# Optimization experiments

Measured on AMD Instinct MI355X. Metric: run time of the kernel, lower is better.

Reference implementation:

```python
import jax, jax.numpy as jnp
import numpy as np

HID = 256
B, H, W, Q = 4, 192, 192, 36864


def conv3x3(x, w, b):
    # x [B,C,H,W], w [O,C,3,3]
    y = jax.lax.conv_general_dilated(x, w, (1, 1), ((1, 1), (1, 1)),
                                     dimension_numbers=('NCHW', 'OIHW', 'NCHW'))
    return y + b[None, :, None, None]


def gather_nchw(x, iy, ix):
    # nearest-neighbor gather: x [B,C,H,W], iy/ix [B,Q] -> [B,Q,C]
    b, c, h, w = x.shape
    lin = iy * w + ix
    g = jnp.take_along_axis(x.reshape(b, c, h * w), lin[:, None, :], axis=2)
    return jnp.transpose(g, (0, 2, 1))


def bilinear_border(x, cy, cx):
    # grid_sample bilinear, padding_mode='border', align_corners=False
    b, c, h, w = x.shape
    fy = ((cy + 1.0) * h - 1.0) * 0.5
    fx = ((cx + 1.0) * w - 1.0) * 0.5
    y0 = jnp.floor(fy)
    x0 = jnp.floor(fx)
    wy = fy - y0
    wx = fx - x0
    y0i = jnp.clip(y0, 0, h - 1).astype(jnp.int32)
    y1i = jnp.clip(y0 + 1, 0, h - 1).astype(jnp.int32)
    x0i = jnp.clip(x0, 0, w - 1).astype(jnp.int32)
    x1i = jnp.clip(x0 + 1, 0, w - 1).astype(jnp.int32)
    v00 = gather_nchw(x, y0i, x0i)
    v01 = gather_nchw(x, y0i, x1i)
    v10 = gather_nchw(x, y1i, x0i)
    v11 = gather_nchw(x, y1i, x1i)
    wy = wy[..., None]
    wx = wx[..., None]
    return (v00 * (1 - wy) * (1 - wx) + v01 * (1 - wy) * wx
            + v10 * wy * (1 - wx) + v11 * wy * wx)


def setup_inputs():
    key = jax.random.key(0)
    ks = jax.random.split(key, 20)
    sc = 0.05
    d = {}
    d['inp'] = jax.random.normal(ks[0], (B, 3, H, W), jnp.float32)
    d['score'] = jax.random.normal(ks[1], (B, 3, H, W), jnp.float32)
    d['coord'] = jax.random.uniform(ks[2], (B, Q, 2), jnp.float32, -1.0, 1.0)
    d['cell'] = jnp.full((B, Q, 2), 2.0 / H, jnp.float32)
    d['coef_w'] = jax.random.normal(ks[3], (HID, 9, 3, 3), jnp.float32) * sc
    d['coef_b'] = jnp.zeros((HID,), jnp.float32)
    d['freq_w'] = jax.random.normal(ks[4], (HID, 9, 3, 3), jnp.float32) * sc
    d['freq_b'] = jnp.zeros((HID,), jnp.float32)
    d['phase_w'] = jax.random.normal(ks[5], (HID // 2, 2), jnp.float32) * sc  # Linear(2, HID//2, bias=False)
    d['a1_w'] = jax.random.normal(ks[6], (128, 3, 3, 3), jnp.float32) * sc
    d['a1_b'] = jnp.zeros((128,), jnp.float32)
    d['a2_w'] = jax.random.normal(ks[7], (3, 128, 3, 3), jnp.float32) * sc
    d['a2_b'] = jnp.zeros((3,), jnp.float32)
    dims = [HID, 256, 256, 256, 256, 3]
    for i in range(5):
        d[f'im_w{i}'] = jax.random.normal(ks[8 + i], (dims[i + 1], dims[i]), jnp.float32) * sc
        d[f'im_b{i}'] = jnp.zeros((dims[i + 1],), jnp.float32)
    return d


def lte_forward(inp, score, coord, cell,
                coef_w, coef_b, freq_w, freq_b, phase_w,
                a1_w, a1_b, a2_w, a2_b,
                im_w0, im_b0, im_w1, im_b1, im_w2, im_b2, im_w3, im_b3, im_w4, im_b4):
    # adapter: conv -> sin -> conv -> sin (Sine w0=1)
    weights = jnp.sin(conv3x3(jnp.sin(conv3x3(inp, a1_w, a1_b)), a2_w, a2_b))
    feat = jnp.concatenate([inp, score, weights], axis=1)  # [B,9,H,W]
    coef = conv3x3(feat, coef_w, coef_b)  # [B,HID,H,W]
    freq = conv3x3(feat, freq_w, freq_b)
    h, w = feat.shape[-2], feat.shape[-1]
    eps = 1e-6
    # single ensemble member (vx=vy=0): clamp coord and nearest-sample
    cy = jnp.clip(coord[..., 0], -1 + eps, 1 - eps)
    cx = jnp.clip(coord[..., 1], -1 + eps, 1 - eps)
    iy = jnp.clip(jnp.round(((cy + 1.0) * h - 1.0) * 0.5), 0, h - 1).astype(jnp.int32)
    ix = jnp.clip(jnp.round(((cx + 1.0) * w - 1.0) * 0.5), 0, w - 1).astype(jnp.int32)
    q_coef = gather_nchw(coef, iy, ix)  # [B,Q,HID]
    q_freq = gather_nchw(freq, iy, ix)  # [B,Q,HID]
    # nearest pixel-center coordinates (make_coord values)
    qy = -1.0 + (2.0 * iy.astype(jnp.float32) + 1.0) / h
    qx = -1.0 + (2.0 * ix.astype(jnp.float32) + 1.0) / w
    rel = jnp.stack([(coord[..., 0] - qy) * h, (coord[..., 1] - qx) * w], axis=-1)  # [B,Q,2]
    rel_cell = cell * jnp.asarray([h, w], jnp.float32)
    # split into (even,odd) frequency pairs: [B,Q,HID/2,2], contract with rel_coord
    qf = q_freq.reshape(q_freq.shape[0], q_freq.shape[1], HID // 2, 2)
    qf = jnp.einsum('bqjk,bqk->bqj', qf, rel)  # [B,Q,HID/2]
    qf = qf + jnp.einsum('bqk,jk->bqj', rel_cell, phase_w)  # phase linear, no bias
    qf = jnp.concatenate([jnp.cos(jnp.pi * qf), jnp.sin(jnp.pi * qf)], axis=-1)  # [B,Q,HID]
    x = q_coef * qf
    for lw, lb in ((im_w0, im_b0), (im_w1, im_b1), (im_w2, im_b2), (im_w3, im_b3)):
        x = jax.nn.relu(jnp.einsum('bqi,oi->bqo', x, lw) + lb)
    pred = jnp.einsum('bqi,oi->bqo', x, im_w4) + im_b4  # [B,Q,3]
    area = jnp.abs(rel[..., 0] * rel[..., 1]) + 1e-9
    ret = pred * (area / area)[..., None]  # single member -> weight 1 (kept for fidelity)
    ret = ret + bilinear_border(inp, coord[..., 0], coord[..., 1])
    return ret


def reference(inp, score, coord, cell,
              coef_w, coef_b, freq_w, freq_b, phase_w,
              a1_w, a1_b, a2_w, a2_b,
              im_w0, im_b0, im_w1, im_b1, im_w2, im_b2, im_w3, im_b3, im_w4, im_b4):
    return lte_forward(inp, score, coord, cell,
                       coef_w, coef_b, freq_w, freq_b, phase_w,
                       a1_w, a1_b, a2_w, a2_b,
                       im_w0, im_b0, im_w1, im_b1, im_w2, im_b2, im_w3, im_b3, im_w4, im_b4)
```

## Files before the change

kernel.cpp:

```cpp
#include <hip/hip_runtime.h>

typedef unsigned short u16;
typedef unsigned int   u32;
typedef unsigned long long u64;
typedef __attribute__((ext_vector_type(8))) short v8s;
typedef __attribute__((ext_vector_type(8))) unsigned short v8u;
typedef __attribute__((ext_vector_type(4))) float v4f;

#define PI_F 3.14159265358979323846f

__device__ __forceinline__ float bf2f(u16 v){ u32 u = ((u32)v) << 16; return __builtin_bit_cast(float, u); }
__device__ __forceinline__ u16 f2bf(float f){
    u32 u = __builtin_bit_cast(u32, f);
    u32 r = (u + 0x7fffu + ((u >> 16) & 1u)) >> 16;
    return (u16)r;
}
__device__ __forceinline__ bool is_f32(const void* cellp){
    u32 u = *(const u32*)cellp;
    return ((u >> 16) != (u & 0xffffu));
}
__device__ __forceinline__ float ldin(const void* p, int i, bool f32){
    return f32 ? ((const float*)p)[i] : bf2f(((const u16*)p)[i]);
}

#define FEAT16_OFF 0
#define W2P_OFF   4718592
#define A1W_OFF   4816896
#define A1B_OFF   4830720
#define A2W_OFF   4831232
#define A2B_OFF   4845056
#define PWF_OFF   4845312
#define IBF_OFF   4846336
#define IWC_OFF   4850688
#define CBP_OFF   5376512
#define W4P_OFF   5378560
#define W1SW_OFF  5386752
#define W2SW_OFF  5403136

__global__ __launch_bounds__(256) void k_pack(
    const void* cw, const void* fw, const void* a1w, const void* a1b,
    const void* a2w, const void* a2b, const void* cb, const void* fb, const void* pwp,
    const void* iw0, const void* ib0, const void* iw1, const void* ib1,
    const void* iw2, const void* ib2, const void* iw3, const void* ib3,
    const void* iw4, const void* ib4, const void* cellp, char* ws){
    bool f32 = is_f32(cellp);
    u16*   w2p  = (u16*)(ws + W2P_OFF);
    float* a1wf = (float*)(ws + A1W_OFF);
    float* a1bf = (float*)(ws + A1B_OFF);
    float* a2wf = (float*)(ws + A2W_OFF);
    float* a2bf = (float*)(ws + A2B_OFF);
    float* pwf  = (float*)(ws + PWF_OFF);
    float* ibf  = (float*)(ws + IBF_OFF);
    u16*   iwc  = (u16*)(ws + IWC_OFF);
    float* cbp  = (float*)(ws + CBP_OFF);
    u16*   w4p  = (u16*)(ws + W4P_OFF);
    u16*   w1sw = (u16*)(ws + W1SW_OFF);
    u16*   w2sw = (u16*)(ws + W2SW_OFF);

    int t = blockIdx.x*256 + threadIdx.x;
    if (t < 49152){
        int c = t >> 9, rem = t & 511;
        int tile = c/3, ks = c%3;
        int lm = rem >> 5, r2 = rem & 31, quad = r2 >> 3, jj = r2 & 7;
        int n = tile*16 + lm;
        int r = quad*8 + jj;
        u16 v = 0;
        if (r < 27){
            int pix = r/9, ch = r%9;
            int tap = ks*3 + pix;
            int src = ch*9 + tap;
            if (n < 256) v = f2bf(ldin(cw, n*81 + src, f32));
            else { int u_ = n - 256; int tt = u_ >> 4, nn = u_ & 15;
                   int f = 2*((tt>>1)*16 + nn) + (tt & 1);
                   v = f2bf(ldin(fw, f*81 + src, f32)); }
        }
        w2p[t] = v; return;
    }
    t -= 49152;
    if (t < 3456){ a1wf[t] = ldin(a1w, t, f32); return; }
    t -= 3456;
    if (t < 128){ a1bf[t] = ldin(a1b, t, f32); return; }
    t -= 128;
    if (t < 3456){
        int o = t/1152, r = t%1152, c = r/9, tap = r%9;
        a2wf[(o*9 + tap)*128 + c] = ldin(a2w, t, f32); return;
    }
    t -= 3456;
    if (t < 3){ a2bf[t] = ldin(a2b, t, f32); return; }
    t -= 3;
    if (t < 256){ pwf[t] = ldin(pwp, t, f32); return; }
    t -= 256;
    if (t < 1027){
        const void* src = (t < 256) ? ib0 : (t < 512) ? ib1 : (t < 768) ? ib2 : (t < 1024) ? ib3 : ib4;
        int idx = (t < 1024) ? (t & 255) : (t - 1024);
        ibf[t] = ldin(src, idx, f32); return;
    }
    t -= 1027;
    if (t < 262144){
        int c = t >> 9, rem = t & 511;
        int lm = rem >> 5, r2 = rem & 31, quad = r2 >> 3, jj = r2 & 7;
        int nt = c & 3, ks = (c >> 2) & 7, wv = (c >> 5) & 3, l = c >> 7;
        int col = wv*64 + nt*16 + lm;
        int k = ks*32 + quad*8 + jj;
        const void* src = (l==0) ? iw0 : (l==1) ? iw1 : (l==2) ? iw2 : iw3;
        iwc[t] = f2bf(ldin(src, col*256 + k, f32)); return;
    }
    t -= 262144;
    if (t < 768){ return; }
    t -= 768;
    if (t < 512){
        float v;
        if (t < 256) v = ldin(cb, t, f32);
        else { int u_ = t - 256; int tt = u_ >> 4, nn = u_ & 15;
               int f = 2*((tt>>1)*16 + nn) + (tt & 1); v = ldin(fb, f, f32); }
        cbp[t] = v; return;
    }
    t -= 512;
    if (t < 4096){
        int ks = t >> 9, rem = t & 511;
        int lm = rem >> 5, r2 = rem & 31, quad = r2 >> 3, jj = r2 & 7;
        int k = ks*32 + quad*8 + jj;
        w4p[t] = (lm < 3) ? f2bf(ldin(iw4, lm*256 + k, f32)) : (u16)0;
        return;
    }
    t -= 4096;
    if (t < 8192){
        int c = t >> 9, rem = t & 511;
        int lm = rem >> 5, r2 = rem & 31, quad = r2 >> 3, jj = r2 & 7;
        int h = c >> 3, nt = (c & 7) >> 1, ks = c & 1;
        int ch = h*64 + nt*16 + lm;
        int kk = quad*8 + jj;
        u16 v = 0;
        int jr = -1, r = 0;
        if (ks == 0){ jr = kk >> 4; r = kk & 15; }
        else if (kk < 16){ jr = 2; r = kk; }
        if (jr >= 0 && r < 12){
            int px = r >> 2, ci = r & 3;
            if (ci < 3) v = f2bf(ldin(a1w, ch*27 + ci*9 + jr*3 + px, f32));
        }
        w1sw[t] = v; return;
    }
    t -= 8192;
    if (t < 18432){
        int c = t >> 9, rem = t & 511;
        int lm = rem >> 5, r2 = rem & 31, quad = r2 >> 3, jj = r2 & 7;
        int h = c / 18, tap = (c % 18) >> 1, ks = c & 1;
        int k = ks*32 + quad*8 + jj;
        int ch = h*64 + k;
        u16 v = 0;
        if (lm < 3) v = f2bf(ldin(a2w, lm*1152 + ch*9 + tap, f32));
        w2sw[t] = v; return;
    }
}

__global__ __launch_bounds__(256, 3) void k_adapter(const void* __restrict__ inp, const void* __restrict__ score,
                                                    const void* __restrict__ cellp, char* __restrict__ ws){
    __shared__ __attribute__((aligned(16))) char smem[46480];
    bool f32 = is_f32(cellp);
    const float* a1bf = (const float*)(ws + A1B_OFF);
    const float* a2bf = (const float*)(ws + A2B_OFF);
    const u16*   w1sw = (const u16*)(ws + W1SW_OFF);
    const u16*   w2sw = (const u16*)(ws + W2SW_OFF);
    u16* feat16 = (u16*)(ws + FEAT16_OFF);

    int blk = blockIdx.x; int b = blk/288; int rem = blk%288;
    int ty0 = (rem/12)*8, tx0 = (rem%12)*16;
    int tid = threadIdx.x;
    u16* S   = (u16*)smem;
    u16* A   = (u16*)(smem + 1920);
    u16* hid = (u16*)(smem + 22000);

    if (tid < 240) ((u64*)smem)[tid] = 0ULL;
    __syncthreads();
    #pragma unroll 1
    for (int e = tid; e < 720; e += 256){
        int ci = e/240, r2 = e%240, hy = r2/20, hx = r2%20;
        int gy = ty0 - 2 + hy, gx = tx0 - 2 + hx;
        if (gy >= 0 && gy < 192 && gx >= 0 && gx < 192)
            S[(hy*20+hx)*4 + ci] = f2bf(ldin(inp, (b*3+ci)*36864 + gy*192 + gx, f32));
    }
    __syncthreads();
    #pragma unroll 1
    for (int p = tid; p < 193; p += 256){
        u64* drow = (u64*)(A + p*52);
        if (p < 180){
            int hy = p/18, hx = p%18;
            #pragma unroll
            for (int jr = 0; jr < 3; ++jr){
                const u64* srow = (const u64*)(S + ((hy+jr)*20 + hx)*4);
                u64 v0 = srow[0], v1 = srow[1], v2 = srow[2];
                drow[jr*4+0] = v0; drow[jr*4+1] = v1; drow[jr*4+2] = v2; drow[jr*4+3] = 0ULL;
            }
            drow[12] = 0ULL;
        } else {
            #pragma unroll
            for (int k = 0; k < 13; ++k) drow[k] = 0ULL;
        }
    }
    __syncthreads();

    const int wv = tid >> 6, ln = tid & 63;
    const int lm = ln & 15, quad = ln >> 4;
    const int laneoff = lm*32 + quad*8;

    float bias2 = (lm < 3) ? a2bf[lm] : 0.f;
    v4f acc2[2];
    acc2[0] = (v4f){bias2,bias2,bias2,bias2};
    acc2[1] = acc2[0];

    #pragma unroll 1
    for (int h = 0; h < 2; ++h){
        float bias1 = a1bf[h*64 + wv*16 + lm];
        v8s B0 = *(const v8s*)(w1sw + (h*8 + wv*2 + 0)*512 + laneoff);
        v8s B1 = *(const v8s*)(w1sw + (h*8 + wv*2 + 1)*512 + laneoff);
        #pragma unroll 4
        for (int mt = 0; mt < 12; ++mt){
            const u16* ar = A + (mt*16 + lm)*52 + quad*8;
            v8s a0 = *(const v8s*)(ar);
            v8s a1 = *(const v8s*)(ar + 32);
            v4f c = (v4f){bias1,bias1,bias1,bias1};
            c = __builtin_amdgcn_mfma_f32_16x16x32_bf16(a0, B0, c, 0,0,0);
            c = __builtin_amdgcn_mfma_f32_16x16x32_bf16(a1, B1, c, 0,0,0);
            #pragma unroll
            for (int r = 0; r < 4; ++r){
                int px = mt*16 + quad*4 + r;
                if (px < 180){
                    int hy = px/18, hx = px - hy*18;
                    int gy = ty0 - 1 + hy, gx = tx0 - 1 + hx;
                    bool ok = (gy >= 0) & (gy < 192) & (gx >= 0) & (gx < 192);
                    hid[px*68 + wv*16 + lm] = ok ? f2bf(__sinf(c[r])) : (u16)0;
                }
            }
        }
        __syncthreads();
        #pragma unroll 2
        for (int tap = 0; tap < 9; ++tap){
            int ty = tap/3, tx = tap%3;
            v8s Bt0 = *(const v8s*)(w2sw + ((h*9 + tap)*2 + 0)*512 + laneoff);
            v8s Bt1 = *(const v8s*)(w2sw + ((h*9 + tap)*2 + 1)*512 + laneoff);
            #pragma unroll
            for (int i = 0; i < 2; ++i){
                int py = wv*2 + i;
                const u16* hrow = hid + ((py+ty)*18 + lm + tx)*68;
                v8s a0 = *(const v8s*)(hrow + quad*8);
                v8s a1 = *(const v8s*)(hrow + 32 + quad*8);
                acc2[i] = __builtin_amdgcn_mfma_f32_16x16x32_bf16(a0, Bt0, acc2[i], 0,0,0);
                acc2[i] = __builtin_amdgcn_mfma_f32_16x16x32_bf16(a1, Bt1, acc2[i], 0,0,0);
            }
        }
        __syncthreads();
    }
    u16* out3 = S;
    if (lm < 3){
        #pragma unroll
        for (int i = 0; i < 2; ++i)
            #pragma unroll
            for (int r = 0; r < 4; ++r){
                int m = (wv*2 + i)*16 + quad*4 + r;
                out3[m*4 + lm] = f2bf(__sinf(acc2[i][r]));
            }
    }
    __syncthreads();
    if (tid < 128){
        int py = tid >> 4, px = tid & 15;
        int gy = ty0 + py, gx = tx0 + px;
        int pi = b*3*36864 + gy*192 + gx;
        v8u lo, hi;
        lo[0] = f2bf(ldin(inp, pi, f32));
        lo[1] = f2bf(ldin(inp, pi + 36864, f32));
        lo[2] = f2bf(ldin(inp, pi + 2*36864, f32));
        lo[3] = f2bf(ldin(score, pi, f32));
        lo[4] = f2bf(ldin(score, pi + 36864, f32));
        lo[5] = f2bf(ldin(score, pi + 2*36864, f32));
        lo[6] = out3[tid*4 + 0];
        lo[7] = out3[tid*4 + 1];
        hi[0] = out3[tid*4 + 2];
        hi[1]=hi[2]=hi[3]=hi[4]=hi[5]=hi[6]=hi[7]=0;
        u16* fp = feat16 + ((b*192 + gy)*192 + gx)*16;
        *(v8u*)fp = lo;
        *(v8u*)(fp + 8) = hi;
    }
}

__global__ __launch_bounds__(256, 3) void k_mega(const char* __restrict__ ws,
                                                 const void* __restrict__ inp,
                                                 const void* __restrict__ coord,
                                                 const void* __restrict__ cellp,
                                                 void* __restrict__ out){
    __shared__ __attribute__((aligned(16))) char smem[46080];
    bool f32 = is_f32(cellp);
    const u16*   feat16 = (const u16*)(ws + FEAT16_OFF);
    const u16*   w2p    = (const u16*)(ws + W2P_OFF);
    const float* pwf    = (const float*)(ws + PWF_OFF);
    const float* ibf    = (const float*)(ws + IBF_OFF);
    const u16*   iwc    = (const u16*)(ws + IWC_OFF);
    const float* cbp    = (const float*)(ws + CBP_OFF);
    const u16*   w4p    = (const u16*)(ws + W4P_OFF);

    const int tid = threadIdx.x;
    const int qg0 = blockIdx.x * 64;
    const int b = qg0 / 36864;

    {
        int q = tid >> 2, j = tid & 3;
        int qg = qg0 + q;
        u16* ap = (u16*)(smem + 32768);
        float c0 = ldin(coord, qg*2, f32), c1 = ldin(coord, qg*2+1, f32);
        const float e = 1e-6f;
        float cy = fminf(fmaxf(c0, -1.f+e), 1.f-e);
        float cx = fminf(fmaxf(c1, -1.f+e), 1.f-e);
        int iy = (int)rintf(((cy+1.f)*192.f-1.f)*0.5f); iy = min(max(iy,0),191);
        int ix = (int)rintf(((cx+1.f)*192.f-1.f)*0.5f); ix = min(max(ix,0),191);
        if (j < 3){
            int yy = iy - 1 + j;
            bool yok = (yy >= 0) & (yy <= 191);
            union { u16 a[32]; v8u v[4]; } buf;
            #pragma unroll
            for (int c = 0; c < 32; ++c) buf.a[c] = 0;
            if (yok){
                const u16* base = feat16 + ((b*192 + yy)*192)*16;
                #pragma unroll
                for (int pix = 0; pix < 3; ++pix){
                    int xx = ix - 1 + pix;
                    if (xx >= 0 && xx <= 191){
                        const u16* s = base + xx*16;
                        v8u v = *(const v8u*)s;
                        u16 c8 = s[8];
                        #pragma unroll
                        for (int c = 0; c < 8; ++c) buf.a[pix*9+c] = v[c];
                        buf.a[pix*9+8] = c8;
                    }
                }
            }
            u16* dst = ap + q*96 + j*32;
            *(v8u*)(dst)      = buf.v[0];
            *(v8u*)(dst + 8)  = buf.v[1];
            *(v8u*)(dst + 16) = buf.v[2];
            *(v8u*)(dst + 24) = buf.v[3];
        } else {
            float qy = -1.f + (2.f*iy + 1.f)/192.f;
            float qx = -1.f + (2.f*ix + 1.f)/192.f;
            float4 mmv;
            mmv.x = (c0 - qy)*192.f; mmv.y = (c1 - qx)*192.f;
            mmv.z = ldin(cellp, qg*2, f32)*192.f; mmv.w = ldin(cellp, qg*2+1, f32)*192.f;
            ((float4*)(smem + 45056))[q] = mmv;
        }
    }
    __syncthreads();

    const int wv = tid >> 6, ln = tid & 63;
    const int lm = ln & 15, quad = ln >> 4;
    const int laneoff = lm*32 + quad*8;
    u16* X = (u16*)smem;

    {
        v8s afr[3];
        #pragma unroll
        for (int ks = 0; ks < 3; ++ks)
            afr[ks] = *(const v8s*)(smem + 32768 + ((wv*16 + lm)*96 + ks*32 + quad*8)*2);
        float4 mm[4];
        #pragma unroll
        for (int r = 0; r < 4; ++r)
            mm[r] = ((const float4*)(smem + 45056))[wv*16 + quad*4 + r];
        float p0[8], p1[8];
        #pragma unroll
        for (int g = 0; g < 8; ++g){
            int j = g*16 + lm;
            p0[g] = pwf[2*j]; p1[g] = pwf[2*j+1];
        }
        v8s Bc0[3], Bc1[3], Bf0[3], Bf1[3];
        {
            const u16* p;
            p = w2p + 0*1536  + laneoff; Bc0[0]=*(const v8s*)p; Bc0[1]=*(const v8s*)(p+512); Bc0[2]=*(const v8s*)(p+1024);
            p = w2p + 8*1536  + laneoff; Bc1[0]=*(const v8s*)p; Bc1[1]=*(const v8s*)(p+512); Bc1[2]=*(const v8s*)(p+1024);
            p = w2p + 16*1536 + laneoff; Bf0[0]=*(const v8s*)p; Bf0[1]=*(const v8s*)(p+512); Bf0[2]=*(const v8s*)(p+1024);
            p = w2p + 17*1536 + laneoff; Bf1[0]=*(const v8s*)p; Bf1[1]=*(const v8s*)(p+512); Bf1[2]=*(const v8s*)(p+1024);
        }
        #pragma unroll 1
        for (int g = 0; g < 8; ++g){
            float bb0 = cbp[g*16+lm], bb1 = cbp[(8+g)*16+lm];
            float bb2 = cbp[(16+2*g)*16+lm], bb3 = cbp[(17+2*g)*16+lm];
            v4f a0 = (v4f){bb0,bb0,bb0,bb0};
            v4f a1 = (v4f){bb1,bb1,bb1,bb1};
            v4f a2 = (v4f){bb2,bb2,bb2,bb2};
            v4f a3 = (v4f){bb3,bb3,bb3,bb3};
            #pragma unroll
            for (int ks = 0; ks < 3; ++ks){
                a0 = __builtin_amdgcn_mfma_f32_16x16x32_bf16(afr[ks], Bc0[ks], a0, 0,0,0);
                a1 = __builtin_amdgcn_mfma_f32_16x16x32_bf16(afr[ks], Bc1[ks], a1, 0,0,0);
                a2 = __builtin_amdgcn_mfma_f32_16x16x32_bf16(afr[ks], Bf0[ks], a2, 0,0,0);
                a3 = __builtin_amdgcn_mfma_f32_16x16x32_bf16(afr[ks], Bf1[ks], a3, 0,0,0);
            }
            if (g < 7){
                const u16* p;
                p = w2p + (g+1)*1536    + laneoff; Bc0[0]=*(const v8s*)p; Bc0[1]=*(const v8s*)(p+512); Bc0[2]=*(const v8s*)(p+1024);
                p = w2p + (9+g)*1536    + laneoff; Bc1[0]=*(const v8s*)p; Bc1[1]=*(const v8s*)(p+512); Bc1[2]=*(const v8s*)(p+1024);
                p = w2p + (18+2*g)*1536 + laneoff; Bf0[0]=*(const v8s*)p; Bf0[1]=*(const v8s*)(p+512); Bf0[2]=*(const v8s*)(p+1024);
                p = w2p + (19+2*g)*1536 + laneoff; Bf1[0]=*(const v8s*)p; Bf1[1]=*(const v8s*)(p+512); Bf1[2]=*(const v8s*)(p+1024);
            }
            int j = g*16 + lm;
            int koff_c = (j>>5)*2048 + (j&31);
            int koff_s = ((128+j)>>5)*2048 + (j&31);
            #pragma unroll
            for (int r = 0; r < 4; ++r){
                float qf = a2[r]*mm[r].x + a3[r]*mm[r].y + mm[r].z*p0[g] + mm[r].w*p1[g];
                float sn, cs;
                __sincosf(PI_F * qf, &sn, &cs);
                int q = wv*16 + quad*4 + r;
                X[koff_c + q*32] = f2bf(a0[r] * cs);
                X[koff_s + q*32] = f2bf(a1[r] * sn);
            }
        }
    }
    __syncthreads();

    #pragma unroll 1
    for (int l = 0; l < 4; ++l){
        const u16* Wb = iwc + (l*4 + wv)*16384 + laneoff;
        v4f acc[4][4];
        #pragma unroll
        for (int nt = 0; nt < 4; ++nt){
            float bv = ibf[l*256 + wv*64 + nt*16 + lm];
            #pragma unroll
            for (int mt = 0; mt < 4; ++mt) acc[nt][mt] = (v4f){bv,bv,bv,bv};
        }
        v8s bw[2][4];
        #pragma unroll
        for (int nt = 0; nt < 4; ++nt){
            bw[0][nt] = *(const v8s*)(Wb + (0*4 + nt)*512);
            bw[1][nt] = *(const v8s*)(Wb + (1*4 + nt)*512);
        }
        #pragma unroll
        for (int ks = 0; ks < 8; ++ks){
            v8s a[4];
            #pragma unroll
            for (int mt = 0; mt < 4; ++mt)
                a[mt] = *(const v8s*)(smem + (ks*2048 + (mt*16 + lm)*32 + quad*8)*2);
            v8s nb[4];
            if (ks < 6){
                #pragma unroll
                for (int nt = 0; nt < 4; ++nt)
                    nb[nt] = *(const v8s*)(Wb + ((ks+2)*4 + nt)*512);
            }
            #pragma unroll
            for (int nt = 0; nt < 4; ++nt)
                #pragma unroll
                for (int mt = 0; mt < 4; ++mt)
                    acc[nt][mt] = __builtin_amdgcn_mfma_f32_16x16x32_bf16(a[mt], bw[ks&1][nt], acc[nt][mt], 0,0,0);
            if (ks < 6){
                #pragma unroll
                for (int nt = 0; nt < 4; ++nt) bw[ks&1][nt] = nb[nt];
            }
        }
        __syncthreads();
        #pragma unroll
        for (int nt = 0; nt < 4; ++nt){
            int col = wv*64 + nt*16 + lm;
            u16* base = X + (col>>5)*2048 + (col&31);
            #pragma unroll
            for (int mt = 0; mt < 4; ++mt)
                #pragma unroll
                for (int r = 0; r < 4; ++r){
                    int q = mt*16 + quad*4 + r;
                    base[q*32] = f2bf(fmaxf(acc[nt][mt][r], 0.f));
                }
        }
        __syncthreads();
    }

    {
        float bv = (lm < 3) ? ibf[1024 + lm] : 0.f;
        v4f accf = (v4f){bv,bv,bv,bv};
        v8s bA = *(const v8s*)(w4p + laneoff);
        #pragma unroll
        for (int ks = 0; ks < 8; ++ks){
            v8s a = *(const v8s*)(smem + (ks*2048 + (wv*16 + lm)*32 + quad*8)*2);
            v8s bN;
            if (ks < 7) bN = *(const v8s*)(w4p + (ks+1)*512 + laneoff);
            accf = __builtin_amdgcn_mfma_f32_16x16x32_bf16(a, bA, accf, 0,0,0);
            bA = bN;
        }
        if (lm < 3){
            #pragma unroll
            for (int r = 0; r < 4; ++r){
                int q = wv*16 + quad*4 + r;
                int qg = qg0 + q;
                float c0 = ldin(coord, qg*2, f32), c1 = ldin(coord, qg*2+1, f32);
                float fy = ((c0 + 1.f)*192.f - 1.f)*0.5f;
                float fx = ((c1 + 1.f)*192.f - 1.f)*0.5f;
                float y0 = floorf(fy), x0 = floorf(fx);
                float wy = fy - y0, wx = fx - x0;
                int y0i = (int)fminf(fmaxf(y0, 0.f), 191.f);
                int y1i = (int)fminf(fmaxf(y0 + 1.f, 0.f), 191.f);
                int x0i = (int)fminf(fmaxf(x0, 0.f), 191.f);
                int x1i = (int)fminf(fmaxf(x0 + 1.f, 0.f), 191.f);
                int ibase = (b*3 + lm)*36864;
                float v00 = ldin(inp, ibase + y0i*192 + x0i, f32);
                float v01 = ldin(inp, ibase + y0i*192 + x1i, f32);
                float v10 = ldin(inp, ibase + y1i*192 + x0i, f32);
                float v11 = ldin(inp, ibase + y1i*192 + x1i, f32);
                float bil = v00*(1.f-wy)*(1.f-wx) + v01*(1.f-wy)*wx + v10*wy*(1.f-wx) + v11*wy*wx;
                float val = accf[r] + bil;
                if (f32) ((float*)out)[qg*3 + lm] = val;
                else     ((u16*)out)[qg*3 + lm] = f2bf(val);
            }
        }
    }
}

extern "C" void kernel_launch(void* const* d_in, const int* in_sizes, int n_in,
                              void* d_out, int out_size, void* d_ws, size_t ws_size,
                              hipStream_t stream){
    (void)in_sizes; (void)n_in; (void)out_size; (void)ws_size;
    const void* inp   = d_in[0];
    const void* score = d_in[1];
    const void* coord = d_in[2];
    const void* cellp = d_in[3];
    const void* cw    = d_in[4];
    const void* cb    = d_in[5];
    const void* fw    = d_in[6];
    const void* fb    = d_in[7];
    const void* pw    = d_in[8];
    const void* a1w   = d_in[9];
    const void* a1b   = d_in[10];
    const void* a2w   = d_in[11];
    const void* a2b   = d_in[12];
    const void* iw0   = d_in[13];
    const void* ib0   = d_in[14];
    const void* iw1   = d_in[15];
    const void* ib1   = d_in[16];
    const void* iw2   = d_in[17];
    const void* ib2   = d_in[18];
    const void* iw3   = d_in[19];
    const void* ib3   = d_in[20];
    const void* iw4   = d_in[21];
    const void* ib4   = d_in[22];
    char* ws = (char*)d_ws;

    hipLaunchKernelGGL(k_pack, dim3(1374), dim3(256), 0, stream,
                       cw, fw, a1w, a1b, a2w, a2b, cb, fb, pw,
                       iw0, ib0, iw1, ib1, iw2, ib2, iw3, ib3, iw4, ib4,
                       cellp, ws);
    hipLaunchKernelGGL(k_adapter, dim3(1152), dim3(256), 0, stream, inp, score, cellp, ws);
    hipLaunchKernelGGL(k_mega, dim3(2304), dim3(256), 0, stream, (const char*)ws, inp, coord, cellp, d_out);
}
```

Baseline: 313.5 us.

## Split MLP GEMM across waves by query rows instead of output columns

The hidden-layer GEMM work is redistributed: each wave now computes all 256 output columns for its own 16 query rows, where before it computed 64 columns for all 64 rows. The weight packing is reordered to match, and the B-fragment stream is double-buffered across 32 groups. This cuts LDS activation reads per wave (one A fragment per k-step instead of four). In exchange every wave streams the full weight matrix from global/L2, four times the weight traffic per block.

```diff
diff --git a/kernel.cpp b/kernel.cpp
--- a/kernel.cpp
+++ b/kernel.cpp
@@ -99,8 +99,8 @@
     if (t < 262144){
         int c = t >> 9, rem = t & 511;
         int lm = rem >> 5, r2 = rem & 31, quad = r2 >> 3, jj = r2 & 7;
-        int nt = c & 3, ks = (c >> 2) & 7, wv = (c >> 5) & 3, l = c >> 7;
-        int col = wv*64 + nt*16 + lm;
+        int nt = c & 15, ks = (c >> 4) & 7, l = c >> 7;
+        int col = nt*16 + lm;
         int k = ks*32 + quad*8 + jj;
         const void* src = (l==0) ? iw0 : (l==1) ? iw1 : (l==2) ? iw2 : iw3;
         iwc[t] = f2bf(ldin(src, col*256 + k, f32)); return;
@@ -416,54 +416,50 @@
 
     #pragma unroll 1
     for (int l = 0; l < 4; ++l){
-        const u16* Wb = iwc + (l*4 + wv)*16384 + laneoff;
-        v4f acc[4][4];
-        #pragma unroll
-        for (int nt = 0; nt < 4; ++nt){
-            float bv = ibf[l*256 + wv*64 + nt*16 + lm];
-            #pragma unroll
-            for (int mt = 0; mt < 4; ++mt) acc[nt][mt] = (v4f){bv,bv,bv,bv};
+        const u16* Wb = iwc + l*65536 + laneoff;
+        v4f acc[16];
+        #pragma unroll
+        for (int nt = 0; nt < 16; ++nt){
+            float bv = ibf[l*256 + nt*16 + lm];
+            acc[nt] = (v4f){bv,bv,bv,bv};
         }
         v8s bw[2][4];
         #pragma unroll
-        for (int nt = 0; nt < 4; ++nt){
-            bw[0][nt] = *(const v8s*)(Wb + (0*4 + nt)*512);
-            bw[1][nt] = *(const v8s*)(Wb + (1*4 + nt)*512);
+        for (int j = 0; j < 4; ++j){
+            bw[0][j] = *(const v8s*)(Wb + (0*4 + j)*512);
+            bw[1][j] = *(const v8s*)(Wb + (1*4 + j)*512);
         }
         #pragma unroll
         for (int ks = 0; ks < 8; ++ks){
-            v8s a[4];
-            #pragma unroll
-            for (int mt = 0; mt < 4; ++mt)
-                a[mt] = *(const v8s*)(smem + (ks*2048 + (mt*16 + lm)*32 + quad*8)*2);
-            v8s nb[4];
-            if (ks < 6){
+            v8s a = *(const v8s*)(smem + (ks*2048 + (wv*16 + lm)*32 + quad*8)*2);
+            #pragma unroll
+            for (int ng = 0; ng < 4; ++ng){
+                int g = ks*4 + ng;
+                v8s nb[4];
+                if (g < 30){
+                    #pragma unroll
+                    for (int j = 0; j < 4; ++j)
+                        nb[j] = *(const v8s*)(Wb + ((g+2)*4 + j)*512);
+                }
                 #pragma unroll
-                for (int nt = 0; nt < 4; ++nt)
-                    nb[nt] = *(const v8s*)(Wb + ((ks+2)*4 + nt)*512);
-            }
-            #pragma unroll
-            for (int nt = 0; nt < 4; ++nt)
-                #pragma unroll
-                for (int mt = 0; mt < 4; ++mt)
-                    acc[nt][mt] = __builtin_amdgcn_mfma_f32_16x16x32_bf16(a[mt], bw[ks&1][nt], acc[nt][mt], 0,0,0);
-            if (ks < 6){
-                #pragma unroll
-                for (int nt = 0; nt < 4; ++nt) bw[ks&1][nt] = nb[nt];
+                for (int j = 0; j < 4; ++j)
+                    acc[ng*4+j] = __builtin_amdgcn_mfma_f32_16x16x32_bf16(a, bw[g&1][j], acc[ng*4+j], 0,0,0);
+                if (g < 30){
+                    #pragma unroll
+                    for (int j = 0; j < 4; ++j) bw[g&1][j] = nb[j];
+                }
             }
         }
         __syncthreads();
         #pragma unroll
-        for (int nt = 0; nt < 4; ++nt){
-            int col = wv*64 + nt*16 + lm;
+        for (int nt = 0; nt < 16; ++nt){
+            int col = nt*16 + lm;
             u16* base = X + (col>>5)*2048 + (col&31);
             #pragma unroll
-            for (int mt = 0; mt < 4; ++mt)
-                #pragma unroll
-                for (int r = 0; r < 4; ++r){
-                    int q = mt*16 + quad*4 + r;
-                    base[q*32] = f2bf(fmaxf(acc[nt][mt][r], 0.f));
-                }
+            for (int r = 0; r < 4; ++r){
+                int q = wv*16 + quad*4 + r;
+                base[q*32] = f2bf(fmaxf(acc[nt][r], 0.f));
+            }
         }
         __syncthreads();
     }
```

After: 498.0 us. 58.9% more time.
